# Kernel tuning notes

Hardware: AMD Instinct MI355X
Metric: run time of the kernel (lower is better)

The kernel has to match this reference:

```python
import jax, jax.numpy as jnp
import numpy as np

TOP_K = 2  # active_experts


def setup_inputs() -> dict:
    key = jax.random.key(0)
    k0, k1, k2, k3 = jax.random.split(key, 4)
    B, S, D, E, H = 4, 1024, 2048, 16, 1024
    x = jax.random.normal(k0, (B, S, D), jnp.float32) * 0.02
    Wg = jax.random.normal(k1, (E, D), jnp.float32) * 0.02          # gate: Linear(dim, E, bias=False)
    balance_bias = jnp.zeros((E,), jnp.float32)                      # registered buffer, init zeros
    W1 = jax.random.normal(k2, (E, D, H), jnp.float32) * 0.02        # expert up-proj (no bias)
    W2 = jax.random.normal(k3, (E, H, D), jnp.float32) * 0.02        # expert down-proj (no bias)
    return {"x": x, "Wg": Wg, "balance_bias": balance_bias, "W1": W1, "W2": W2}


def reference(x, Wg, balance_bias, W1, W2):
    B, S, D = x.shape
    E = Wg.shape[0]
    xf = x.reshape(-1, D)                                   # [T, D], T = B*S
    T = xf.shape[0]

    # sigmoid gating with load-balance bias
    gate_logits = xf @ Wg.T                                 # [T, E]
    gate_scores = jax.nn.sigmoid(gate_logits + balance_bias)

    # top-k selection + normalization (matches torch.topk + sum-normalize)
    topk_scores, topk_idx = jax.lax.top_k(gate_scores, TOP_K)
    topk_scores = topk_scores / (topk_scores.sum(-1, keepdims=True) + 1e-6)

    # dense combine weights [T, E]: zero for unselected experts -> identical math
    # to the per-expert masked index_add in the original module
    combine = jnp.zeros((T, E), xf.dtype).at[jnp.arange(T)[:, None], topk_idx].add(topk_scores)

    # per-expert FFN: SiLU(x W1_e) W2_e, weighted-combined across experts
    h = jax.nn.silu(jnp.einsum('td,edh->teh', xf, W1))      # [T, E, H]
    out = jnp.einsum('teh,te,ehd->td', h, combine, W2)      # [T, D]
    return out.reshape(B, S, D)
```

## Files before the change

kernel.cpp:

```cpp
#include <hip/hip_runtime.h>
#include <math.h>

#define T_TOK 4096
#define DDIM  2048
#define HDIM  1024
#define NEXP  16
#define CAP   4096
#define GBM   128
#define GBN   128
#define GBK   64
#define MAX_TILES 80

typedef __attribute__((ext_vector_type(8))) short  short8;
typedef __attribute__((ext_vector_type(4))) float  floatx4;

__device__ __forceinline__ unsigned short f2bf(float f) {
    unsigned int u = __float_as_uint(f);
    u += 0x7fffu + ((u >> 16) & 1u);
    return (unsigned short)(u >> 16);
}
__device__ __forceinline__ float bf2f(unsigned short u) {
    return __uint_as_float((unsigned int)u << 16);
}

__device__ __forceinline__ void gl_lds16(const void* g, void* l) {
    __builtin_amdgcn_global_load_lds(
        (const __attribute__((address_space(1))) unsigned int*)g,
        (__attribute__((address_space(3))) unsigned int*)l,
        16, 0, 0);
}

__global__ __launch_bounds__(256) void prep_kernel(
    const float* __restrict__ x, const float* __restrict__ Wg,
    const float* __restrict__ bias,
    const float* __restrict__ W1, const float* __restrict__ W2,
    unsigned short* __restrict__ W1T, unsigned short* __restrict__ W2T,
    int* __restrict__ counts, int* __restrict__ tok_list,
    int4* __restrict__ tinfo, float2* __restrict__ wcomb,
    unsigned short* __restrict__ xbf)
{
    __shared__ __align__(16) unsigned short Ls[64 * 256];
    int z   = blockIdx.z;
    int bid = blockIdx.x;
    int tid = threadIdx.x;

    if (bid < 128) {
        const float* src; unsigned short* dst; int K, N, kt, nt;
        if (z < NEXP) {
            K = DDIM; N = HDIM;
            src = W1 + (size_t)z * K * N;
            dst = W1T + (size_t)z * (size_t)N * K;
            kt = bid >> 4; nt = bid & 15;
        } else {
            K = HDIM; N = DDIM;
            src = W2 + (size_t)(z - NEXP) * K * N;
            dst = W2T + (size_t)(z - NEXP) * (size_t)N * K;
            kt = bid >> 5; nt = bid & 31;
        }
        int kb = kt * 256, nb = nt * 64;
        int r = tid >> 4;
        int c16 = tid & 15;
        const float* s0 = src + (size_t)kb * N + nb + c16 * 4;

#pragma unroll
        for (int i4 = 0; i4 < 4; ++i4) {
            float4 v[4];
#pragma unroll
            for (int i = 0; i < 4; ++i)
                v[i] = *(const float4*)(s0 + (size_t)(i4 * 64 + r * 4 + i) * N);
#pragma unroll
            for (int j = 0; j < 4; ++j) {
                unsigned int lo = (unsigned int)f2bf(((const float*)&v[0])[j])
                                | ((unsigned int)f2bf(((const float*)&v[1])[j]) << 16);
                unsigned int hi = (unsigned int)f2bf(((const float*)&v[2])[j])
                                | ((unsigned int)f2bf(((const float*)&v[3])[j]) << 16);
                int n  = c16 * 4 + j;
                int g  = i4 * 16 + r;
                int gp = g ^ (n & 14);
                *(uint2*)&Ls[n * 256 + gp * 4] = make_uint2(lo, hi);
            }
        }
        __syncthreads();
        unsigned short* d0 = dst + (size_t)nb * K + kb;
#pragma unroll
        for (int j = 0; j < 8; ++j) {
            int c = tid + j * 256;
            int n = c >> 5, a = c & 31;
            int sp = (2 * a) ^ (n & 14);
            short8 sv = *(const short8*)&Ls[n * 256 + sp * 4];
            *(short8*)(d0 + (size_t)n * K + a * 8) = sv;
        }
        return;
    }

    int gb   = z * 8 + (bid - 128);
    int wv   = tid >> 6;
    int lane = tid & 63;
    const float4* wg4 = (const float4*)Wg;

    for (int tk = 0; tk < 4; ++tk) {
        int t = gb * 16 + wv * 4 + tk;

        const float4* xp4 = (const float4*)x + (size_t)t * (DDIM / 4);
        ushort4* xbp4 = (ushort4*)(xbf + (size_t)t * DDIM);

        float acc[NEXP];
#pragma unroll
        for (int e = 0; e < NEXP; ++e) acc[e] = 0.f;

        for (int it = 0; it < DDIM / 4 / 64; ++it) {
            int d4 = it * 64 + lane;
            float4 xv = xp4[d4];
            ushort4 xs;
            xs.x = f2bf(xv.x); xs.y = f2bf(xv.y);
            xs.z = f2bf(xv.z); xs.w = f2bf(xv.w);
            xbp4[d4] = xs;
#pragma unroll
            for (int e = 0; e < NEXP; ++e) {
                float4 wvv = wg4[e * (DDIM / 4) + d4];
                acc[e] += xv.x * wvv.x + xv.y * wvv.y + xv.z * wvv.z + xv.w * wvv.w;
            }
        }
#pragma unroll
        for (int e = 0; e < NEXP; ++e) {
            float v = acc[e];
#pragma unroll
            for (int off = 32; off > 0; off >>= 1) v += __shfl_xor(v, off, 64);
            acc[e] = v;
        }
        if (lane == 0) {
            float s[NEXP];
#pragma unroll
            for (int e = 0; e < NEXP; ++e)
                s[e] = 1.f / (1.f + expf(-(acc[e] + bias[e])));
            int i0 = 0;
#pragma unroll
            for (int e = 1; e < NEXP; ++e) if (s[e] > s[i0]) i0 = e;
            int i1 = (i0 == 0) ? 1 : 0;
            for (int e = 0; e < NEXP; ++e)
                if (e != i0 && s[e] > s[i1]) i1 = e;
            float denom = s[i0] + s[i1] + 1e-6f;
            int p0 = atomicAdd(&counts[i0], 1);
            tok_list[i0 * CAP + p0] = t;
            int p1 = atomicAdd(&counts[i1], 1);
            tok_list[i1 * CAP + p1] = t;
            tinfo[t] = make_int4(i0, p0, i1, p1);
            wcomb[t] = make_float2(s[i0] / denom, s[i1] / denom);
        }
    }
}

__global__ void scan_kernel(const int* __restrict__ counts, int* __restrict__ offsets,
                            int* __restrict__ ntiles, int* __restrict__ tile_e,
                            int* __restrict__ tile_mt)
{
    int lane = threadIdx.x;
    int c = (lane < NEXP) ? counts[lane] : 0;
    int incl = c;
#pragma unroll
    for (int d = 1; d < 64; d <<= 1) {
        int v = __shfl_up(incl, d, 64);
        if (lane >= d) incl += v;
    }
    if (lane < NEXP) offsets[lane] = incl - c;
    if (lane == NEXP - 1) offsets[NEXP] = incl;

    int nt_e = (lane < NEXP) ? ((c + GBM - 1) / GBM) : 0;
    int tincl = nt_e;
#pragma unroll
    for (int d = 1; d < 64; d <<= 1) {
        int v = __shfl_up(tincl, d, 64);
        if (lane >= d) tincl += v;
    }
    int tbase = tincl - nt_e;
    if (lane < NEXP) {
        for (int i = 0; i < nt_e; ++i) {
            tile_e[tbase + i]  = lane;
            tile_mt[tbase + i] = i;
        }
        if (lane == NEXP - 1) *ntiles = tbase + nt_e;
    }
}

__global__ __launch_bounds__(256) void up_gemm(
    const unsigned short* __restrict__ xbf, const unsigned short* __restrict__ W1T,
    const int* __restrict__ counts, const int* __restrict__ offsets,
    const int* __restrict__ ntiles, const int* __restrict__ tile_e,
    const int* __restrict__ tile_mt,
    const int* __restrict__ tok_list, unsigned short* __restrict__ hbuf)
{
    int idx = blockIdx.x;
    if (idx >= *ntiles) return;
    int e   = tile_e[idx];
    int mt  = tile_mt[idx];
    int cnt = counts[e];
    int nbase = blockIdx.y * GBN;

    __shared__ __align__(16) unsigned short As[2][GBM * GBK];
    __shared__ __align__(16) unsigned short Bs[2][GBN * GBK];

    int tid = threadIdx.x, lane = tid & 63, wv = tid >> 6;
    int kcL = ((lane & 7) ^ ((lane >> 3) & 7)) * 8;
    int hbase = offsets[e];

    const unsigned short* gA[4];
    const unsigned short* gB[4];
#pragma unroll
    for (int j = 0; j < 4; ++j) {
        int row = wv * 32 + j * 8 + (lane >> 3);
        int m = mt * GBM + row; if (m >= cnt) m = cnt - 1;
        int tok = tok_list[e * CAP + m];
        gA[j] = xbf + (size_t)tok * DDIM + kcL;
        gB[j] = W1T + ((size_t)e * HDIM + nbase + row) * DDIM + kcL;
    }
    int fr = lane & 15, fq = lane >> 4;
    int wm = (wv & 1) * 64, wn = (wv >> 1) * 64;

    floatx4 acc[4][4];
#pragma unroll
    for (int i = 0; i < 4; ++i)
#pragma unroll
        for (int j = 0; j < 4; ++j) acc[i][j] = (floatx4){0.f, 0.f, 0.f, 0.f};

#pragma unroll
    for (int j = 0; j < 4; ++j)
        gl_lds16(gA[j], &As[0][((wv * 4 + j) * 64 + lane) * 8]);
#pragma unroll
    for (int j = 0; j < 4; ++j)
        gl_lds16(gB[j], &Bs[0][((wv * 4 + j) * 64 + lane) * 8]);

    const int NK = DDIM / GBK;
    for (int i = 0; i < NK; ++i) {
        int cur = i & 1, nxt = cur ^ 1;
        __syncthreads();
        if (i + 1 < NK) {
            int k0 = (i + 1) * GBK;
#pragma unroll
            for (int j = 0; j < 4; ++j)
                gl_lds16(gA[j] + k0, &As[nxt][((wv * 4 + j) * 64 + lane) * 8]);
#pragma unroll
            for (int j = 0; j < 4; ++j)
                gl_lds16(gB[j] + k0, &Bs[nxt][((wv * 4 + j) * 64 + lane) * 8]);
        }
#pragma unroll
        for (int ks = 0; ks < 2; ++ks) {
            short8 af[4], bfr[4];
#pragma unroll
            for (int mi = 0; mi < 4; ++mi) {
                int row = wm + mi * 16 + fr;
                int kcs = (ks * 4 + fq) ^ (row & 7);
                af[mi] = *(const short8*)&As[cur][row * GBK + kcs * 8];
            }
#pragma unroll
            for (int ni = 0; ni < 4; ++ni) {
                int row = wn + ni * 16 + fr;
                int kcs = (ks * 4 + fq) ^ (row & 7);
                bfr[ni] = *(const short8*)&Bs[cur][row * GBK + kcs * 8];
            }
#pragma unroll
            for (int mi = 0; mi < 4; ++mi)
#pragma unroll
                for (int ni = 0; ni < 4; ++ni)
                    acc[mi][ni] = __builtin_amdgcn_mfma_f32_16x16x32_bf16(
                        af[mi], bfr[ni], acc[mi][ni], 0, 0, 0);
        }
    }

#pragma unroll
    for (int mi = 0; mi < 4; ++mi) {
#pragma unroll
        for (int r = 0; r < 4; ++r) {
            int row = wm + mi * 16 + fq * 4 + r;
            int m = mt * GBM + row;
            if (m < cnt) {
                size_t ro = (size_t)(hbase + m) * HDIM + nbase + wn;
#pragma unroll
                for (int ni = 0; ni < 4; ++ni) {
                    float u  = acc[mi][ni][r];
                    float hh = u / (1.f + __expf(-u));
                    hbuf[ro + ni * 16 + fr] = f2bf(hh);
                }
            }
        }
    }
}

__global__ __launch_bounds__(256) void down_gemm(
    const unsigned short* __restrict__ hbuf, const unsigned short* __restrict__ W2T,
    const int* __restrict__ counts, const int* __restrict__ offsets,
    const int* __restrict__ ntiles, const int* __restrict__ tile_e,
    const int* __restrict__ tile_mt,
    unsigned short* __restrict__ ybuf)
{
    int idx = blockIdx.x;
    if (idx >= *ntiles) return;
    int e   = tile_e[idx];
    int mt  = tile_mt[idx];
    int cnt = counts[e];
    int nbase = blockIdx.y * GBN;

    __shared__ __align__(16) unsigned short As[2][GBM * GBK];
    __shared__ __align__(16) unsigned short Bs[2][GBN * GBK];

    int tid = threadIdx.x, lane = tid & 63, wv = tid >> 6;
    int kcL = ((lane & 7) ^ ((lane >> 3) & 7)) * 8;
    int hbase = offsets[e];

    const unsigned short* gA[4];
    const unsigned short* gB[4];
#pragma unroll
    for (int j = 0; j < 4; ++j) {
        int row = wv * 32 + j * 8 + (lane >> 3);
        int m = mt * GBM + row; if (m >= cnt) m = cnt - 1;
        gA[j] = hbuf + (size_t)(hbase + m) * HDIM + kcL;
        gB[j] = W2T + ((size_t)e * DDIM + nbase + row) * HDIM + kcL;
    }
    int fr = lane & 15, fq = lane >> 4;
    int wm = (wv & 1) * 64, wn = (wv >> 1) * 64;

    floatx4 acc[4][4];
#pragma unroll
    for (int i = 0; i < 4; ++i)
#pragma unroll
        for (int j = 0; j < 4; ++j) acc[i][j] = (floatx4){0.f, 0.f, 0.f, 0.f};

#pragma unroll
    for (int j = 0; j < 4; ++j)
        gl_lds16(gA[j], &As[0][((wv * 4 + j) * 64 + lane) * 8]);
#pragma unroll
    for (int j = 0; j < 4; ++j)
        gl_lds16(gB[j], &Bs[0][((wv * 4 + j) * 64 + lane) * 8]);

    const int NK = HDIM / GBK;
    for (int i = 0; i < NK; ++i) {
        int cur = i & 1, nxt = cur ^ 1;
        __syncthreads();
        if (i + 1 < NK) {
            int k0 = (i + 1) * GBK;
#pragma unroll
            for (int j = 0; j < 4; ++j)
                gl_lds16(gA[j] + k0, &As[nxt][((wv * 4 + j) * 64 + lane) * 8]);
#pragma unroll
            for (int j = 0; j < 4; ++j)
                gl_lds16(gB[j] + k0, &Bs[nxt][((wv * 4 + j) * 64 + lane) * 8]);
        }
#pragma unroll
        for (int ks = 0; ks < 2; ++ks) {
            short8 af[4], bfr[4];
#pragma unroll
            for (int mi = 0; mi < 4; ++mi) {
                int row = wm + mi * 16 + fr;
                int kcs = (ks * 4 + fq) ^ (row & 7);
                af[mi] = *(const short8*)&As[cur][row * GBK + kcs * 8];
            }
#pragma unroll
            for (int ni = 0; ni < 4; ++ni) {
                int row = wn + ni * 16 + fr;
                int kcs = (ks * 4 + fq) ^ (row & 7);
                bfr[ni] = *(const short8*)&Bs[cur][row * GBK + kcs * 8];
            }
#pragma unroll
            for (int mi = 0; mi < 4; ++mi)
#pragma unroll
                for (int ni = 0; ni < 4; ++ni)
                    acc[mi][ni] = __builtin_amdgcn_mfma_f32_16x16x32_bf16(
                        af[mi], bfr[ni], acc[mi][ni], 0, 0, 0);
        }
    }

#pragma unroll
    for (int mi = 0; mi < 4; ++mi) {
#pragma unroll
        for (int r = 0; r < 4; ++r) {
            int row = wm + mi * 16 + fq * 4 + r;
            int m = mt * GBM + row;
            if (m < cnt) {
                size_t ro = (size_t)(hbase + m) * DDIM + nbase + wn;
#pragma unroll
                for (int ni = 0; ni < 4; ++ni)
                    ybuf[ro + ni * 16 + fr] = f2bf(acc[mi][ni][r]);
            }
        }
    }
}

__global__ __launch_bounds__(256) void combine_kernel(
    const unsigned short* __restrict__ ybuf, const int* __restrict__ offsets,
    const int4* __restrict__ tinfo, const float2* __restrict__ wcomb,
    float* __restrict__ out)
{
    int t = blockIdx.x;
    int4   ti = tinfo[t];
    float2 w  = wcomb[t];
    int s0 = offsets[ti.x] + ti.y;
    int s1 = offsets[ti.z] + ti.w;
    const ushort4* y0 = (const ushort4*)(ybuf + (size_t)s0 * DDIM);
    const ushort4* y1 = (const ushort4*)(ybuf + (size_t)s1 * DDIM);
    float4* op = (float4*)(out + (size_t)t * DDIM);
#pragma unroll
    for (int i = 0; i < 2; ++i) {
        int c = threadIdx.x + i * 256;
        ushort4 a = y0[c], b = y1[c];
        float4 r;
        r.x = w.x * bf2f(a.x) + w.y * bf2f(b.x);
        r.y = w.x * bf2f(a.y) + w.y * bf2f(b.y);
        r.z = w.x * bf2f(a.z) + w.y * bf2f(b.z);
        r.w = w.x * bf2f(a.w) + w.y * bf2f(b.w);
        op[c] = r;
    }
}

extern "C" void kernel_launch(void* const* d_in, const int* in_sizes, int n_in,
                              void* d_out, int out_size, void* d_ws, size_t ws_size,
                              hipStream_t stream)
{
    const float* x    = (const float*)d_in[0];
    const float* Wg   = (const float*)d_in[1];
    const float* bias = (const float*)d_in[2];
    const float* W1   = (const float*)d_in[3];
    const float* W2   = (const float*)d_in[4];
    float* out = (float*)d_out;

    char* ws = (char*)d_ws;
    int*            counts   = (int*)(ws + 0);
    int*            offsets  = (int*)(ws + 256);
    int*            ntiles   = (int*)(ws + 512);
    int*            tile_e   = (int*)(ws + 512 + 4);
    int*            tile_mt  = (int*)(ws + 512 + 4 + MAX_TILES * 4);
    int*            tok_list = (int*)(ws + 2048);
    int4*           tinfo    = (int4*)(ws + 264192);
    float2*         wcomb    = (float2*)(ws + 329728);
    unsigned short* xbf      = (unsigned short*)(ws + 524288);
    unsigned short* hbuf     = (unsigned short*)(ws + 17301504);
    unsigned short* ybuf     = (unsigned short*)(ws + 34078720);
    unsigned short* W1T      = (unsigned short*)(ws + 67633152);
    unsigned short* W2T      = (unsigned short*)(ws + 134742016);

    hipMemsetAsync(counts, 0, 64, stream);

    prep_kernel<<<dim3(136, 1, 32), 256, 0, stream>>>(
        x, Wg, bias, W1, W2, W1T, W2T, counts, tok_list, tinfo, wcomb, xbf);
    scan_kernel<<<1, 64, 0, stream>>>(counts, offsets, ntiles, tile_e, tile_mt);
    up_gemm<<<dim3(MAX_TILES, HDIM / GBN), 256, 0, stream>>>(
        xbf, W1T, counts, offsets, ntiles, tile_e, tile_mt, tok_list, hbuf);
    down_gemm<<<dim3(MAX_TILES, DDIM / GBN), 256, 0, stream>>>(
        hbuf, W2T, counts, offsets, ntiles, tile_e, tile_mt, ybuf);
    combine_kernel<<<T_TOK, 256, 0, stream>>>(ybuf, offsets, tinfo, wcomb, out);
}
```

Baseline: 647.7 us.

## Pack expert weights in k-octet layout and swizzle GEMM block order

Replaces the transposing weight prep with a simpler conversion that packs each group of 8 K-rows into contiguous 16-byte chunks per column. The GEMM B-tiles then load straight from this layout and read LDS without an XOR swizzle. It also splits gating into its own kernel and remaps the GEMM grid to 1D with a swizzled order so that co-resident blocks share weight tiles in cache. The risk is LDS bank conflicts in the new B read pattern and a conversion kernel with strided 16-byte writes.

```diff
diff --git a/kernel.cpp b/kernel.cpp
--- a/kernel.cpp
+++ b/kernel.cpp
@@ -30,123 +30,104 @@
         16, 0, 0);
 }
 
-__global__ __launch_bounds__(256) void prep_kernel(
+__global__ __launch_bounds__(256) void wconv_kernel(
+    const float* __restrict__ W1, const float* __restrict__ W2,
+    unsigned short* __restrict__ W1p, unsigned short* __restrict__ W2p)
+{
+    __shared__ __align__(16) unsigned short Lp[8 * 2048];
+    int bid = blockIdx.x;
+    const float* src; unsigned short* dst; int N;
+    if (bid < 4096) {
+        int e = bid >> 8, oct = bid & 255;
+        src = W1  + ((size_t)e * 2048 + oct * 8) * 1024;
+        dst = W1p + ((size_t)e * 2048 + oct * 8) * 1024;
+        N = 1024;
+    } else {
+        int b2 = bid - 4096;
+        int e = b2 >> 7, oct = b2 & 127;
+        src = W2  + ((size_t)e * 1024 + oct * 8) * 2048;
+        dst = W2p + ((size_t)e * 1024 + oct * 8) * 2048;
+        N = 2048;
+    }
+    int t = threadIdx.x;
+    int r = t >> 5, l32 = t & 31;
+
+    for (int i = 0; i < N / 128; ++i) {
+        int c4 = l32 + i * 32;
+        float4 v = *(const float4*)(src + (size_t)r * N + c4 * 4);
+        ushort4 s;
+        s.x = f2bf(v.x); s.y = f2bf(v.y); s.z = f2bf(v.z); s.w = f2bf(v.w);
+        *(ushort4*)&Lp[r * N + c4 * 4] = s;
+    }
+    __syncthreads();
+
+    for (int q = 0; q < N / 256; ++q) {
+        int n = t + q * 256;
+        short8 o;
+#pragma unroll
+        for (int r8 = 0; r8 < 8; ++r8) o[r8] = (short)Lp[r8 * N + n];
+        *(short8*)(dst + (size_t)n * 8) = o;
+    }
+}
+
+__global__ __launch_bounds__(256) void gate_kernel(
     const float* __restrict__ x, const float* __restrict__ Wg,
     const float* __restrict__ bias,
-    const float* __restrict__ W1, const float* __restrict__ W2,
-    unsigned short* __restrict__ W1T, unsigned short* __restrict__ W2T,
     int* __restrict__ counts, int* __restrict__ tok_list,
     int4* __restrict__ tinfo, float2* __restrict__ wcomb,
     unsigned short* __restrict__ xbf)
 {
-    __shared__ __align__(16) unsigned short Ls[64 * 256];
-    int z   = blockIdx.z;
-    int bid = blockIdx.x;
-    int tid = threadIdx.x;
-
-    if (bid < 128) {
-        const float* src; unsigned short* dst; int K, N, kt, nt;
-        if (z < NEXP) {
-            K = DDIM; N = HDIM;
-            src = W1 + (size_t)z * K * N;
-            dst = W1T + (size_t)z * (size_t)N * K;
-            kt = bid >> 4; nt = bid & 15;
-        } else {
-            K = HDIM; N = DDIM;
-            src = W2 + (size_t)(z - NEXP) * K * N;
-            dst = W2T + (size_t)(z - NEXP) * (size_t)N * K;
-            kt = bid >> 5; nt = bid & 31;
-        }
-        int kb = kt * 256, nb = nt * 64;
-        int r = tid >> 4;
-        int c16 = tid & 15;
-        const float* s0 = src + (size_t)kb * N + nb + c16 * 4;
-
-#pragma unroll
-        for (int i4 = 0; i4 < 4; ++i4) {
-            float4 v[4];
-#pragma unroll
-            for (int i = 0; i < 4; ++i)
-                v[i] = *(const float4*)(s0 + (size_t)(i4 * 64 + r * 4 + i) * N);
-#pragma unroll
-            for (int j = 0; j < 4; ++j) {
-                unsigned int lo = (unsigned int)f2bf(((const float*)&v[0])[j])
-                                | ((unsigned int)f2bf(((const float*)&v[1])[j]) << 16);
-                unsigned int hi = (unsigned int)f2bf(((const float*)&v[2])[j])
-                                | ((unsigned int)f2bf(((const float*)&v[3])[j]) << 16);
-                int n  = c16 * 4 + j;
-                int g  = i4 * 16 + r;
-                int gp = g ^ (n & 14);
-                *(uint2*)&Ls[n * 256 + gp * 4] = make_uint2(lo, hi);
-            }
-        }
-        __syncthreads();
-        unsigned short* d0 = dst + (size_t)nb * K + kb;
-#pragma unroll
-        for (int j = 0; j < 8; ++j) {
-            int c = tid + j * 256;
-            int n = c >> 5, a = c & 31;
-            int sp = (2 * a) ^ (n & 14);
-            short8 sv = *(const short8*)&Ls[n * 256 + sp * 4];
-            *(short8*)(d0 + (size_t)n * K + a * 8) = sv;
-        }
-        return;
-    }
-
-    int gb   = z * 8 + (bid - 128);
-    int wv   = tid >> 6;
-    int lane = tid & 63;
+    int tb   = blockIdx.x;
+    int wv   = threadIdx.x >> 6;
+    int lane = threadIdx.x & 63;
+    int t    = tb * 4 + wv;
+
+    const float4* xp4 = (const float4*)x + (size_t)t * (DDIM / 4);
+    ushort4* xbp4 = (ushort4*)(xbf + (size_t)t * DDIM);
     const float4* wg4 = (const float4*)Wg;
 
-    for (int tk = 0; tk < 4; ++tk) {
-        int t = gb * 16 + wv * 4 + tk;
-
-        const float4* xp4 = (const float4*)x + (size_t)t * (DDIM / 4);
-        ushort4* xbp4 = (ushort4*)(xbf + (size_t)t * DDIM);
-
-        float acc[NEXP];
-#pragma unroll
-        for (int e = 0; e < NEXP; ++e) acc[e] = 0.f;
-
-        for (int it = 0; it < DDIM / 4 / 64; ++it) {
-            int d4 = it * 64 + lane;
-            float4 xv = xp4[d4];
-            ushort4 xs;
-            xs.x = f2bf(xv.x); xs.y = f2bf(xv.y);
-            xs.z = f2bf(xv.z); xs.w = f2bf(xv.w);
-            xbp4[d4] = xs;
-#pragma unroll
-            for (int e = 0; e < NEXP; ++e) {
-                float4 wvv = wg4[e * (DDIM / 4) + d4];
-                acc[e] += xv.x * wvv.x + xv.y * wvv.y + xv.z * wvv.z + xv.w * wvv.w;
-            }
-        }
+    float acc[NEXP];
+#pragma unroll
+    for (int e = 0; e < NEXP; ++e) acc[e] = 0.f;
+
+    for (int it = 0; it < DDIM / 4 / 64; ++it) {
+        int d4 = it * 64 + lane;
+        float4 xv = xp4[d4];
+        ushort4 xs;
+        xs.x = f2bf(xv.x); xs.y = f2bf(xv.y);
+        xs.z = f2bf(xv.z); xs.w = f2bf(xv.w);
+        xbp4[d4] = xs;
 #pragma unroll
         for (int e = 0; e < NEXP; ++e) {
-            float v = acc[e];
-#pragma unroll
-            for (int off = 32; off > 0; off >>= 1) v += __shfl_xor(v, off, 64);
-            acc[e] = v;
-        }
-        if (lane == 0) {
-            float s[NEXP];
-#pragma unroll
-            for (int e = 0; e < NEXP; ++e)
-                s[e] = 1.f / (1.f + expf(-(acc[e] + bias[e])));
-            int i0 = 0;
-#pragma unroll
-            for (int e = 1; e < NEXP; ++e) if (s[e] > s[i0]) i0 = e;
-            int i1 = (i0 == 0) ? 1 : 0;
-            for (int e = 0; e < NEXP; ++e)
-                if (e != i0 && s[e] > s[i1]) i1 = e;
-            float denom = s[i0] + s[i1] + 1e-6f;
-            int p0 = atomicAdd(&counts[i0], 1);
-            tok_list[i0 * CAP + p0] = t;
-            int p1 = atomicAdd(&counts[i1], 1);
-            tok_list[i1 * CAP + p1] = t;
-            tinfo[t] = make_int4(i0, p0, i1, p1);
-            wcomb[t] = make_float2(s[i0] / denom, s[i1] / denom);
-        }
+            float4 wvv = wg4[e * (DDIM / 4) + d4];
+            acc[e] += xv.x * wvv.x + xv.y * wvv.y + xv.z * wvv.z + xv.w * wvv.w;
+        }
+    }
+#pragma unroll
+    for (int e = 0; e < NEXP; ++e) {
+        float v = acc[e];
+#pragma unroll
+        for (int off = 32; off > 0; off >>= 1) v += __shfl_xor(v, off, 64);
+        acc[e] = v;
+    }
+    if (lane == 0) {
+        float s[NEXP];
+#pragma unroll
+        for (int e = 0; e < NEXP; ++e)
+            s[e] = 1.f / (1.f + expf(-(acc[e] + bias[e])));
+        int i0 = 0;
+#pragma unroll
+        for (int e = 1; e < NEXP; ++e) if (s[e] > s[i0]) i0 = e;
+        int i1 = (i0 == 0) ? 1 : 0;
+        for (int e = 0; e < NEXP; ++e)
+            if (e != i0 && s[e] > s[i1]) i1 = e;
+        float denom = s[i0] + s[i1] + 1e-6f;
+        int p0 = atomicAdd(&counts[i0], 1);
+        tok_list[i0 * CAP + p0] = t;
+        int p1 = atomicAdd(&counts[i1], 1);
+        tok_list[i1 * CAP + p1] = t;
+        tinfo[t] = make_int4(i0, p0, i1, p1);
+        wcomb[t] = make_float2(s[i0] / denom, s[i1] / denom);
     }
 }
 
@@ -182,19 +163,22 @@
     }
 }
 
+
 __global__ __launch_bounds__(256) void up_gemm(
-    const unsigned short* __restrict__ xbf, const unsigned short* __restrict__ W1T,
+    const unsigned short* __restrict__ xbf, const unsigned short* __restrict__ W1p,
     const int* __restrict__ counts, const int* __restrict__ offsets,
     const int* __restrict__ ntiles, const int* __restrict__ tile_e,
     const int* __restrict__ tile_mt,
     const int* __restrict__ tok_list, unsigned short* __restrict__ hbuf)
 {
-    int idx = blockIdx.x;
+    int w = blockIdx.x;
+    int swz = (w & 7) * 80 + (w >> 3);
+    int idx = swz >> 3;
+    int nbase = (swz & 7) * GBN;
     if (idx >= *ntiles) return;
     int e   = tile_e[idx];
     int mt  = tile_mt[idx];
     int cnt = counts[e];
-    int nbase = blockIdx.y * GBN;
 
     __shared__ __align__(16) unsigned short As[2][GBM * GBK];
     __shared__ __align__(16) unsigned short Bs[2][GBN * GBK];
@@ -204,15 +188,23 @@
     int hbase = offsets[e];
 
     const unsigned short* gA[4];
-    const unsigned short* gB[4];
 #pragma unroll
     for (int j = 0; j < 4; ++j) {
         int row = wv * 32 + j * 8 + (lane >> 3);
         int m = mt * GBM + row; if (m >= cnt) m = cnt - 1;
         int tok = tok_list[e * CAP + m];
         gA[j] = xbf + (size_t)tok * DDIM + kcL;
-        gB[j] = W1T + ((size_t)e * HDIM + nbase + row) * DDIM + kcL;
-    }
+    }
+
+    const unsigned short* gB[4];
+#pragma unroll
+    for (int j = 0; j < 4; ++j) {
+        int s = wv * 4 + j;
+        gB[j] = W1p + (size_t)e * DDIM * HDIM
+              + ((size_t)(s >> 1) * HDIM + nbase + (s & 1) * 64 + lane) * 8;
+    }
+    const size_t kstepB = (size_t)GBK * HDIM;
+
     int fr = lane & 15, fq = lane >> 4;
     int wm = (wv & 1) * 64, wn = (wv >> 1) * 64;
 
@@ -240,7 +232,8 @@
                 gl_lds16(gA[j] + k0, &As[nxt][((wv * 4 + j) * 64 + lane) * 8]);
 #pragma unroll
             for (int j = 0; j < 4; ++j)
-                gl_lds16(gB[j] + k0, &Bs[nxt][((wv * 4 + j) * 64 + lane) * 8]);
+                gl_lds16(gB[j] + (size_t)(i + 1) * kstepB,
+                         &Bs[nxt][((wv * 4 + j) * 64 + lane) * 8]);
         }
 #pragma unroll
         for (int ks = 0; ks < 2; ++ks) {
@@ -254,8 +247,7 @@
 #pragma unroll
             for (int ni = 0; ni < 4; ++ni) {
                 int row = wn + ni * 16 + fr;
-                int kcs = (ks * 4 + fq) ^ (row & 7);
-                bfr[ni] = *(const short8*)&Bs[cur][row * GBK + kcs * 8];
+                bfr[ni] = *(const short8*)&Bs[cur][((ks * 4 + fq) * GBN + row) * 8];
             }
 #pragma unroll
             for (int mi = 0; mi < 4; ++mi)
@@ -286,18 +278,20 @@
 }
 
 __global__ __launch_bounds__(256) void down_gemm(
-    const unsigned short* __restrict__ hbuf, const unsigned short* __restrict__ W2T,
+    const unsigned short* __restrict__ hbuf, const unsigned short* __restrict__ W2p,
     const int* __restrict__ counts, const int* __restrict__ offsets,
     const int* __restrict__ ntiles, const int* __restrict__ tile_e,
     const int* __restrict__ tile_mt,
     unsigned short* __restrict__ ybuf)
 {
-    int idx = blockIdx.x;
+    int w = blockIdx.x;
+    int swz = (w & 7) * 160 + (w >> 3);
+    int idx = swz >> 4;
+    int nbase = (swz & 15) * GBN;
     if (idx >= *ntiles) return;
     int e   = tile_e[idx];
     int mt  = tile_mt[idx];
     int cnt = counts[e];
-    int nbase = blockIdx.y * GBN;
 
     __shared__ __align__(16) unsigned short As[2][GBM * GBK];
     __shared__ __align__(16) unsigned short Bs[2][GBN * GBK];
@@ -307,14 +301,22 @@
     int hbase = offsets[e];
 
     const unsigned short* gA[4];
-    const unsigned short* gB[4];
 #pragma unroll
     for (int j = 0; j < 4; ++j) {
         int row = wv * 32 + j * 8 + (lane >> 3);
         int m = mt * GBM + row; if (m >= cnt) m = cnt - 1;
         gA[j] = hbuf + (size_t)(hbase + m) * HDIM + kcL;
-        gB[j] = W2T + ((size_t)e * DDIM + nbase + row) * HDIM + kcL;
-    }
+    }
+
+    const unsigned short* gB[4];
+#pragma unroll
+    for (int j = 0; j < 4; ++j) {
+        int s = wv * 4 + j;
+        gB[j] = W2p + (size_t)e * HDIM * DDIM
+              + ((size_t)(s >> 1) * DDIM + nbase + (s & 1) * 64 + lane) * 8;
+    }
+    const size_t kstepB = (size_t)GBK * DDIM;
+
     int fr = lane & 15, fq = lane >> 4;
     int wm = (wv & 1) * 64, wn = (wv >> 1) * 64;
 
@@ -342,7 +344,8 @@
                 gl_lds16(gA[j] + k0, &As[nxt][((wv * 4 + j) * 64 + lane) * 8]);
 #pragma unroll
             for (int j = 0; j < 4; ++j)
-                gl_lds16(gB[j] + k0, &Bs[nxt][((wv * 4 + j) * 64 + lane) * 8]);
+                gl_lds16(gB[j] + (size_t)(i + 1) * kstepB,
+                         &Bs[nxt][((wv * 4 + j) * 64 + lane) * 8]);
         }
 #pragma unroll
         for (int ks = 0; ks < 2; ++ks) {
@@ -356,8 +359,7 @@
 #pragma unroll
             for (int ni = 0; ni < 4; ++ni) {
                 int row = wn + ni * 16 + fr;
-                int kcs = (ks * 4 + fq) ^ (row & 7);
-                bfr[ni] = *(const short8*)&Bs[cur][row * GBK + kcs * 8];
+                bfr[ni] = *(const short8*)&Bs[cur][((ks * 4 + fq) * GBN + row) * 8];
             }
 #pragma unroll
             for (int mi = 0; mi < 4; ++mi)
@@ -433,17 +435,18 @@
     unsigned short* xbf      = (unsigned short*)(ws + 524288);
     unsigned short* hbuf     = (unsigned short*)(ws + 17301504);
     unsigned short* ybuf     = (unsigned short*)(ws + 34078720);
-    unsigned short* W1T      = (unsigned short*)(ws + 67633152);
-    unsigned short* W2T      = (unsigned short*)(ws + 134742016);
+    unsigned short* W1p      = (unsigned short*)(ws + 67633152);
+    unsigned short* W2p      = (unsigned short*)(ws + 134742016);
 
     hipMemsetAsync(counts, 0, 64, stream);
 
-    prep_kernel<<<dim3(136, 1, 32), 256, 0, stream>>>(
-        x, Wg, bias, W1, W2, W1T, W2T, counts, tok_list, tinfo, wcomb, xbf);
+    gate_kernel<<<dim3(T_TOK / 4), 256, 0, stream>>>(
+        x, Wg, bias, counts, tok_list, tinfo, wcomb, xbf);
+    wconv_kernel<<<dim3(4096 + 2048), 256, 0, stream>>>(W1, W2, W1p, W2p);
     scan_kernel<<<1, 64, 0, stream>>>(counts, offsets, ntiles, tile_e, tile_mt);
-    up_gemm<<<dim3(MAX_TILES, HDIM / GBN), 256, 0, stream>>>(
-        xbf, W1T, counts, offsets, ntiles, tile_e, tile_mt, tok_list, hbuf);
-    down_gemm<<<dim3(MAX_TILES, DDIM / GBN), 256, 0, stream>>>(
-        hbuf, W2T, counts, offsets, ntiles, tile_e, tile_mt, ybuf);
+    up_gemm<<<dim3(MAX_TILES * 8), 256, 0, stream>>>(
+        xbf, W1p, counts, offsets, ntiles, tile_e, tile_mt, tok_list, hbuf);
+    down_gemm<<<dim3(MAX_TILES * 16), 256, 0, stream>>>(
+        hbuf, W2p, counts, offsets, ntiles, tile_e, tile_mt, ybuf);
     combine_kernel<<<T_TOK, 256, 0, stream>>>(ybuf, offsets, tinfo, wcomb, out);
 }
```

Result: faster. 631.4 us (-2.5%).
